# Kernel tuning notes

Measured on AMD Instinct MI355X. Metric: run time of the kernel, lower is better.

The kernel has to match this reference:

```python
import jax, jax.numpy as jnp
import numpy as np

N_NODES = 50000
N_EDGES = 1600000
N_GRAPHS = 128
IN_C, HID, N_CLS = 128, 256, 10


def setup_inputs() -> dict:
    key = jax.random.key(0)
    ks = jax.random.split(key, 8)
    x = jax.random.normal(ks[0], (N_NODES, IN_C), dtype=jnp.float32)
    edge_index = jax.random.randint(ks[1], (2, N_EDGES), 0, N_NODES, dtype=jnp.int64)
    batch = jnp.sort(jax.random.randint(ks[2], (N_NODES,), 0, N_GRAPHS, dtype=jnp.int64))
    def glorot(k, shape):
        lim = np.sqrt(6.0 / (shape[0] + shape[1]))
        return jax.random.uniform(k, shape, jnp.float32, -lim, lim)
    return {
        "x": x, "edge_index": edge_index, "batch": batch,
        "W1": glorot(ks[3], (IN_C, HID)), "b1": jnp.zeros((HID,), jnp.float32),
        "W2": glorot(ks[4], (HID, HID)), "b2": jnp.zeros((HID,), jnp.float32),
        "Wl1": glorot(ks[5], (HID, 64)), "bl1": jnp.zeros((64,), jnp.float32),
        "Wl2": glorot(ks[6], (64, N_CLS)), "bl2": jnp.zeros((N_CLS,), jnp.float32),
    }


def _gcn_conv(x, row, col, deg_inv_sqrt, W, b):
    h = x @ W                                  # [N, out]
    norm = deg_inv_sqrt[row] * deg_inv_sqrt[col]   # [E]
    msg = h[row] * norm[:, None]                   # gather + scale
    agg = jax.ops.segment_sum(msg, col, num_segments=x.shape[0])
    agg = agg + h * (deg_inv_sqrt * deg_inv_sqrt)[:, None]  # self-loop term (norm = 1/deg)
    return agg + b


def reference(x, edge_index, batch, W1, b1, W2, b2, Wl1, bl1, Wl2, bl2):
    N = x.shape[0]
    row, col = edge_index[0], edge_index[1]
    # degree including self-loop, computed on target nodes (PyG convention)
    deg = jax.ops.segment_sum(jnp.ones((row.shape[0],), x.dtype), col, num_segments=N) + 1.0
    deg_inv_sqrt = jax.lax.rsqrt(deg)

    h = jax.nn.relu(_gcn_conv(x, row, col, deg_inv_sqrt, W1, b1))
    h = jax.nn.relu(_gcn_conv(h, row, col, deg_inv_sqrt, W2, b2))

    # global_mean_pool over batch ids
    sums = jax.ops.segment_sum(h, batch, num_segments=N_GRAPHS)
    cnts = jax.ops.segment_sum(jnp.ones((N,), h.dtype), batch, num_segments=N_GRAPHS)
    g = sums / jnp.maximum(cnts, 1.0)[:, None]     # [G, HID]

    g = jax.nn.relu(g @ Wl1 + bl1)
    return jax.nn.log_softmax(g @ Wl2 + bl2, axis=1)
```

## Files before the change

### kernel.cpp

```cpp
#include <hip/hip_runtime.h>
#include <hip/hip_bf16.h>
#include <math.h>

#define NN 50000
#define NG 128
#define INC 128
#define HIDC 256
#define NCLS 10

#define NBLK 256
#define BSH 8
#define NB 196

typedef __attribute__((ext_vector_type(8))) short s8_t;
typedef __attribute__((ext_vector_type(4))) float f4_t;

__device__ inline f4_t mfma16(s8_t a, s8_t b, f4_t c) {
  return __builtin_amdgcn_mfma_f32_16x16x32_bf16(a, b, c, 0, 0, 0);
}

__device__ inline float bf2f(ushort u) {
  union { unsigned int i; float f; } c; c.i = ((unsigned int)u) << 16; return c.f;
}
__device__ inline ushort f2bf(float f) {
  __hip_bfloat16 h = __float2bfloat16(f);
  return *(ushort*)&h;
}

__device__ inline void gload_lds16(const void* g, void* l) {
  __builtin_amdgcn_global_load_lds(
      (const __attribute__((address_space(1))) unsigned int*)g,
      (__attribute__((address_space(3))) unsigned int*)l, 16, 0, 0);
}

__global__ __launch_bounds__(256) void edge_hist(const int* __restrict__ ecol,
                                                 int* __restrict__ hist, int E, int chunk) {
  __shared__ int h[NB];
  int blk = blockIdx.x;
  for (int i = threadIdx.x; i < NB; i += 256) h[i] = 0;
  __syncthreads();
  int e0 = blk * chunk, e1 = min(e0 + chunk, E);
  for (int e = e0 + threadIdx.x; e < e1; e += 256)
    atomicAdd(&h[ecol[e] >> BSH], 1);
  __syncthreads();
  for (int i = threadIdx.x; i < NB; i += 256) hist[i * NBLK + blk] = h[i];
}

__global__ __launch_bounds__(256) void edge_partition(const int* __restrict__ erow,
                                                      const int* __restrict__ ecol,
                                                      const int* __restrict__ histBase,
                                                      unsigned* __restrict__ part,
                                                      int E, int chunk) {
  __shared__ int cur[NB];
  int blk = blockIdx.x;
  for (int i = threadIdx.x; i < NB; i += 256) cur[i] = histBase[i * NBLK + blk];
  __syncthreads();
  int e0 = blk * chunk, e1 = min(e0 + chunk, E);
  for (int e = e0 + threadIdx.x; e < e1; e += 256) {
    int c = ecol[e];
    int b = c >> BSH;
    int pos = atomicAdd(&cur[b], 1);
    part[pos] = ((unsigned)erow[e] << 8) | (unsigned)(c & 255);
  }
}

__global__ __launch_bounds__(256) void bucket_deg_dis(const unsigned* __restrict__ part,
                                                      const int* __restrict__ histBase,
                                                      int* __restrict__ deg,
                                                      float* __restrict__ dis, int N) {
  __shared__ int cnt[256];
  int b = blockIdx.x;
  cnt[threadIdx.x] = 0;
  __syncthreads();
  int s0 = histBase[b * NBLK];
  int s1 = histBase[(b + 1) * NBLK];
  for (int e = s0 + threadIdx.x; e < s1; e += 256)
    atomicAdd(&cnt[part[e] & 255], 1);
  __syncthreads();
  int node = (b << BSH) + threadIdx.x;
  if (node < N) {
    int d = cnt[threadIdx.x];
    deg[node] = d;
    dis[node] = rsqrtf((float)d + 1.0f);
  }
}

__global__ __launch_bounds__(256) void bucket_csr(const unsigned* __restrict__ part,
                                                  const int* __restrict__ histBase,
                                                  const int* __restrict__ offsets,
                                                  int* __restrict__ rows_csr, int N) {
  __shared__ int cur[256];
  int b = blockIdx.x;
  int node = (b << BSH) + threadIdx.x;
  cur[threadIdx.x] = (node < N) ? offsets[node] : 0;
  __syncthreads();
  int s0 = histBase[b * NBLK];
  int s1 = histBase[(b + 1) * NBLK];
  for (int e = s0 + threadIdx.x; e < s1; e += 256) {
    unsigned pv = part[e];
    int pos = atomicAdd(&cur[pv & 255], 1);
    rows_csr[pos] = (int)(pv >> 8);
  }
}

#define SCAN_T 256
#define SCAN_V 8
#define SCAN_VPB (SCAN_T * SCAN_V)

__global__ __launch_bounds__(SCAN_T) void scanA(const int* __restrict__ deg,
                                                int* __restrict__ offsets,
                                                int* __restrict__ blockTotals, int n) {
  __shared__ int sm[SCAN_T];
  int b = blockIdx.x;
  int t = threadIdx.x;
  int base = b * SCAN_VPB + t * SCAN_V;
  int v[SCAN_V];
  int run = 0;
  #pragma unroll
  for (int j = 0; j < SCAN_V; ++j) {
    int idx = base + j;
    int d = (idx < n) ? deg[idx] : 0;
    run += d;
    v[j] = run;
  }
  sm[t] = run;
  __syncthreads();
  #pragma unroll
  for (int off = 1; off < SCAN_T; off <<= 1) {
    int x = (t >= off) ? sm[t - off] : 0;
    __syncthreads();
    sm[t] += x;
    __syncthreads();
  }
  int excl = (t == 0) ? 0 : sm[t - 1];
  #pragma unroll
  for (int j = 0; j < SCAN_V; ++j) {
    int idx = base + j;
    if (idx < n) offsets[idx + 1] = v[j] + excl;
  }
  if (t == SCAN_T - 1) blockTotals[b] = sm[t];
}

__global__ void scanB(int* __restrict__ blockTotals, int nb) {
  if (threadIdx.x == 0 && blockIdx.x == 0) {
    int run = 0;
    for (int i = 0; i < nb; ++i) {
      int v = blockTotals[i];
      blockTotals[i] = run;
      run += v;
    }
  }
}

__global__ void scanC(int* __restrict__ offsets, const int* __restrict__ blockTotals, int n) {
  int stride = gridDim.x * blockDim.x;
  for (int i = blockIdx.x * blockDim.x + threadIdx.x; i < n; i += stride) {
    offsets[i + 1] += blockTotals[i / SCAN_VPB];
    if (i == 0) offsets[0] = 0;
  }
}

__global__ void cast_f32_bf16(const float* __restrict__ in, ushort* __restrict__ out, int n4) {
  int i = blockIdx.x * blockDim.x + threadIdx.x;
  if (i < n4) {
    float4 v = ((const float4*)in)[i];
    ushort4 o;
    o.x = f2bf(v.x); o.y = f2bf(v.y); o.z = f2bf(v.z); o.w = f2bf(v.w);
    ((ushort4*)out)[i] = o;
  }
}

__global__ void transpose_cast2(const float* __restrict__ W1, ushort* __restrict__ W1T,
                                const float* __restrict__ W2, ushort* __restrict__ W2T) {
  int idx = blockIdx.x * blockDim.x + threadIdx.x;
  if (idx < INC * HIDC) {
    int k = idx / HIDC, n = idx % HIDC;
    W1T[(long)n * INC + k] = f2bf(W1[idx]);
  }
  int i2 = idx - INC * HIDC;
  if (i2 >= 0 && i2 < HIDC * HIDC) {
    int k = i2 / HIDC, n = i2 % HIDC;
    W2T[(long)n * HIDC + k] = f2bf(W2[i2]);
  }
}

__global__ __launch_bounds__(256) void aggregate128_bf16(
    const ushort* __restrict__ xb, const float* __restrict__ dis,
    const int* __restrict__ offsets, const int* __restrict__ rows_csr,
    ushort* __restrict__ outb, int N) {
  int node = blockIdx.x * 4 + (threadIdx.x >> 6);
  if (node >= N) return;
  int lane = threadIdx.x & 63;
  float di = dis[node];
  const unsigned int* xv = (const unsigned int*)xb;
  unsigned int sv = xv[(long)node * 64 + lane];
  float a0 = bf2f((ushort)sv) * di * di;
  float a1 = bf2f((ushort)(sv >> 16)) * di * di;
  int e0 = offsets[node], e1 = offsets[node + 1];
  int e = e0;
  for (; e + 3 < e1; e += 4) {
    int r0 = rows_csr[e], r1 = rows_csr[e + 1];
    int r2 = rows_csr[e + 2], r3 = rows_csr[e + 3];
    float s0 = dis[r0] * di, s1 = dis[r1] * di;
    float s2 = dis[r2] * di, s3 = dis[r3] * di;
    unsigned int v0 = xv[(long)r0 * 64 + lane];
    unsigned int v1 = xv[(long)r1 * 64 + lane];
    unsigned int v2 = xv[(long)r2 * 64 + lane];
    unsigned int v3 = xv[(long)r3 * 64 + lane];
    a0 = fmaf(bf2f((ushort)v0), s0, a0); a1 = fmaf(bf2f((ushort)(v0 >> 16)), s0, a1);
    a0 = fmaf(bf2f((ushort)v1), s1, a0); a1 = fmaf(bf2f((ushort)(v1 >> 16)), s1, a1);
    a0 = fmaf(bf2f((ushort)v2), s2, a0); a1 = fmaf(bf2f((ushort)(v2 >> 16)), s2, a1);
    a0 = fmaf(bf2f((ushort)v3), s3, a0); a1 = fmaf(bf2f((ushort)(v3 >> 16)), s3, a1);
  }
  for (; e < e1; ++e) {
    int r0 = rows_csr[e];
    float s0 = dis[r0] * di;
    unsigned int v0 = xv[(long)r0 * 64 + lane];
    a0 = fmaf(bf2f((ushort)v0), s0, a0); a1 = fmaf(bf2f((ushort)(v0 >> 16)), s0, a1);
  }
  unsigned int o = (unsigned int)f2bf(a0) | ((unsigned int)f2bf(a1) << 16);
  ((unsigned int*)outb)[(long)node * 64 + lane] = o;
}

__global__ __launch_bounds__(256) void aggregate256_bf16(
    const ushort* __restrict__ xb, const float* __restrict__ dis,
    const int* __restrict__ offsets, const int* __restrict__ rows_csr,
    ushort* __restrict__ outb, int N) {
  int node = blockIdx.x * 4 + (threadIdx.x >> 6);
  if (node >= N) return;
  int lane = threadIdx.x & 63;
  float di = dis[node];
  const uint2* xv = (const uint2*)xb;
  uint2 sv = xv[(long)node * 64 + lane];
  float a0 = bf2f((ushort)sv.x) * di * di;
  float a1 = bf2f((ushort)(sv.x >> 16)) * di * di;
  float a2 = bf2f((ushort)sv.y) * di * di;
  float a3 = bf2f((ushort)(sv.y >> 16)) * di * di;
  int e0 = offsets[node], e1 = offsets[node + 1];
  int e = e0;
  for (; e + 3 < e1; e += 4) {
    int r0 = rows_csr[e], r1 = rows_csr[e + 1];
    int r2 = rows_csr[e + 2], r3 = rows_csr[e + 3];
    float s0 = dis[r0] * di, s1 = dis[r1] * di;
    float s2 = dis[r2] * di, s3 = dis[r3] * di;
    uint2 v0 = xv[(long)r0 * 64 + lane];
    uint2 v1 = xv[(long)r1 * 64 + lane];
    uint2 v2 = xv[(long)r2 * 64 + lane];
    uint2 v3 = xv[(long)r3 * 64 + lane];
    a0 = fmaf(bf2f((ushort)v0.x), s0, a0); a1 = fmaf(bf2f((ushort)(v0.x >> 16)), s0, a1);
    a2 = fmaf(bf2f((ushort)v0.y), s0, a2); a3 = fmaf(bf2f((ushort)(v0.y >> 16)), s0, a3);
    a0 = fmaf(bf2f((ushort)v1.x), s1, a0); a1 = fmaf(bf2f((ushort)(v1.x >> 16)), s1, a1);
    a2 = fmaf(bf2f((ushort)v1.y), s1, a2); a3 = fmaf(bf2f((ushort)(v1.y >> 16)), s1, a3);
    a0 = fmaf(bf2f((ushort)v2.x), s2, a0); a1 = fmaf(bf2f((ushort)(v2.x >> 16)), s2, a1);
    a2 = fmaf(bf2f((ushort)v2.y), s2, a2); a3 = fmaf(bf2f((ushort)(v2.y >> 16)), s2, a3);
    a0 = fmaf(bf2f((ushort)v3.x), s3, a0); a1 = fmaf(bf2f((ushort)(v3.x >> 16)), s3, a1);
    a2 = fmaf(bf2f((ushort)v3.y), s3, a2); a3 = fmaf(bf2f((ushort)(v3.y >> 16)), s3, a3);
  }
  for (; e < e1; ++e) {
    int r0 = rows_csr[e];
    float s0 = dis[r0] * di;
    uint2 v0 = xv[(long)r0 * 64 + lane];
    a0 = fmaf(bf2f((ushort)v0.x), s0, a0); a1 = fmaf(bf2f((ushort)(v0.x >> 16)), s0, a1);
    a2 = fmaf(bf2f((ushort)v0.y), s0, a2); a3 = fmaf(bf2f((ushort)(v0.y >> 16)), s0, a3);
  }
  uint2 o;
  o.x = (unsigned int)f2bf(a0) | ((unsigned int)f2bf(a1) << 16);
  o.y = (unsigned int)f2bf(a2) | ((unsigned int)f2bf(a3) << 16);
  ((uint2*)outb)[(long)node * 64 + lane] = o;
}

template <int K>
__global__ __launch_bounds__(256) void gemm_mfma(
    const ushort* __restrict__ A, const ushort* __restrict__ WT,
    const float* __restrict__ bias, ushort* __restrict__ outb, int M) {
  __shared__ ushort smem[24576];
  const int tid = threadIdx.x;
  const int lane = tid & 63;
  const int wave = tid >> 6;
  const int wm = wave >> 1, wn = wave & 1;
  const int m0 = blockIdx.x * 128;

  f4_t acc[4][8] = {};

  for (int k0 = 0; k0 < K; k0 += 64) {
    __syncthreads();
    #pragma unroll
    for (int is = 0; is < 4; ++is) {
      int s = is * 256 + tid;
      int row = s >> 3;
      int ch = (s & 7) ^ (row & 7);
      long grow = m0 + row; if (grow > M - 1) grow = M - 1;
      gload_lds16(A + grow * K + k0 + ch * 8, &smem[(is * 256 + wave * 64) * 8]);
    }
    #pragma unroll
    for (int ib = 0; ib < 8; ++ib) {
      int s = ib * 256 + tid;
      int row = s >> 3;
      int ch = (s & 7) ^ (row & 7);
      gload_lds16(WT + (long)row * K + k0 + ch * 8,
                  &smem[8192 + (ib * 256 + wave * 64) * 8]);
    }
    asm volatile("s_waitcnt vmcnt(0)" ::: "memory");
    __syncthreads();
    #pragma unroll
    for (int ks = 0; ks < 2; ++ks) {
      s8_t af[4];
      #pragma unroll
      for (int mi = 0; mi < 4; ++mi) {
        int row = wm * 64 + mi * 16 + (lane & 15);
        int ch = (ks * 4 + (lane >> 4)) ^ (row & 7);
        af[mi] = *(const s8_t*)(&smem[row * 64 + ch * 8]);
      }
      #pragma unroll
      for (int ni = 0; ni < 8; ++ni) {
        int brow = wn * 128 + ni * 16 + (lane & 15);
        int ch = (ks * 4 + (lane >> 4)) ^ (brow & 7);
        s8_t bf = *(const s8_t*)(&smem[8192 + brow * 64 + ch * 8]);
        #pragma unroll
        for (int mi = 0; mi < 4; ++mi)
          acc[mi][ni] = mfma16(af[mi], bf, acc[mi][ni]);
      }
    }
  }
  #pragma unroll
  for (int ni = 0; ni < 8; ++ni) {
    int col = wn * 128 + ni * 16 + (lane & 15);
    float bb = bias[col];
    #pragma unroll
    for (int mi = 0; mi < 4; ++mi) {
      #pragma unroll
      for (int r = 0; r < 4; ++r) {
        int row = m0 + wm * 64 + mi * 16 + (lane >> 4) * 4 + r;
        if (row < M) {
          float v = fmaxf(acc[mi][ni][r] + bb, 0.0f);
          outb[(long)row * HIDC + col] = f2bf(v);
        }
      }
    }
  }
}

__global__ void find_bounds(const int* __restrict__ batch, int* __restrict__ gstart, int n) {
  int stride = gridDim.x * blockDim.x;
  for (int i = blockIdx.x * blockDim.x + threadIdx.x; i < n; i += stride) {
    int b = batch[i];
    if (i == 0) {
      for (int g = 0; g <= b; ++g) gstart[g] = 0;
    } else {
      int pb = batch[i - 1];
      if (pb != b)
        for (int g = pb + 1; g <= b; ++g) gstart[g] = i;
    }
    if (i == n - 1) {
      for (int g = b + 1; g <= NG; ++g) gstart[g] = n;
    }
  }
}

#define POOL_SPLIT 8
__global__ __launch_bounds__(HIDC) void pool_range_bf16(const ushort* __restrict__ h,
                                                        const int* __restrict__ gstart,
                                                        float* __restrict__ gsum) {
  int g = blockIdx.x;
  int s = blockIdx.y;
  int c = threadIdx.x;
  int s0 = gstart[g], s1 = gstart[g + 1];
  int len = s1 - s0;
  int chunk = (len + POOL_SPLIT - 1) / POOL_SPLIT;
  int i0 = s0 + s * chunk;
  int i1 = min(i0 + chunk, s1);
  float acc = 0.0f;
  for (int i = i0; i < i1; ++i) acc += bf2f(h[(long)i * HIDC + c]);
  if (i1 > i0) atomicAdd(&gsum[g * HIDC + c], acc);
}

__global__ __launch_bounds__(64) void mlp_kernel(
    const float* __restrict__ gsum, const int* __restrict__ gstart,
    const float* __restrict__ Wl1, const float* __restrict__ bl1,
    const float* __restrict__ Wl2, const float* __restrict__ bl2,
    float* __restrict__ out) {
  __shared__ float g[HIDC];
  __shared__ float hid[64];
  __shared__ float logits[NCLS];
  __shared__ float red[2];
  int i = blockIdx.x;
  int t = threadIdx.x;
  int cnt = gstart[i + 1] - gstart[i];
  float inv = 1.0f / fmaxf((float)cnt, 1.0f);
  for (int c = t; c < HIDC; c += 64) g[c] = gsum[i * HIDC + c] * inv;
  __syncthreads();
  float acc = bl1[t];
  for (int c = 0; c < HIDC; ++c) acc = fmaf(g[c], Wl1[c * 64 + t], acc);
  hid[t] = fmaxf(acc, 0.0f);
  __syncthreads();
  if (t < NCLS) {
    float l = bl2[t];
    for (int c = 0; c < 64; ++c) l = fmaf(hid[c], Wl2[c * NCLS + t], l);
    logits[t] = l;
  }
  __syncthreads();
  if (t == 0) {
    float m = -1e30f;
    for (int k = 0; k < NCLS; ++k) m = fmaxf(m, logits[k]);
    float s = 0.f;
    for (int k = 0; k < NCLS; ++k) s += expf(logits[k] - m);
    red[0] = m;
    red[1] = logf(s);
  }
  __syncthreads();
  if (t < NCLS) out[i * NCLS + t] = logits[t] - red[0] - red[1];
}

extern "C" void kernel_launch(void* const* d_in, const int* in_sizes, int n_in,
                              void* d_out, int out_size, void* d_ws, size_t ws_size,
                              hipStream_t stream) {
  const float* x = (const float*)d_in[0];
  const int* edge_index = (const int*)d_in[1];
  const int* batch = (const int*)d_in[2];
  const float* W1 = (const float*)d_in[3];
  const float* b1 = (const float*)d_in[4];
  const float* W2 = (const float*)d_in[5];
  const float* b2 = (const float*)d_in[6];
  const float* Wl1 = (const float*)d_in[7];
  const float* bl1 = (const float*)d_in[8];
  const float* Wl2 = (const float*)d_in[9];
  const float* bl2 = (const float*)d_in[10];
  float* out = (float*)d_out;

  const int N = in_sizes[0] / INC;
  const int E = in_sizes[1] / 2;
  const int* erow = edge_index;
  const int* ecol = edge_index + E;

  char* p = (char*)d_ws;
  auto alloc = [&](size_t bytes) {
    void* r = (void*)p;
    p += (bytes + 255) & ~(size_t)255;
    return r;
  };
  int* deg = (int*)alloc((size_t)N * 4);
  float* dis = (float*)alloc((size_t)N * 4);
  int* offsets = (int*)alloc((size_t)(N + 1) * 4);
  int* rows_csr = (int*)alloc((size_t)E * 4);
  unsigned* part = (unsigned*)alloc((size_t)E * 4);
  int* hist = (int*)alloc((size_t)(NB * NBLK) * 4);
  int* histBase = (int*)alloc((size_t)(NB * NBLK + 1) * 4);
  float* gsum = (float*)alloc((size_t)NG * HIDC * 4);
  int* gstart = (int*)alloc((size_t)(NG + 1) * 4);
  int* blockTotals = (int*)alloc((size_t)256 * 4);
  ushort* W1T = (ushort*)alloc((size_t)INC * HIDC * 2);
  ushort* W2T = (ushort*)alloc((size_t)HIDC * HIDC * 2);
  ushort* xb = (ushort*)alloc((size_t)N * INC * 2);
  ushort* agg1b = (ushort*)alloc((size_t)N * INC * 2);
  ushort* h1b = (ushort*)alloc((size_t)N * HIDC * 2);
  ushort* agg2b = (ushort*)alloc((size_t)N * HIDC * 2);
  ushort* h2b = xb;

  hipMemsetAsync(gsum, 0, (size_t)NG * HIDC * 4, stream);

  const int chunk = (E + NBLK - 1) / NBLK;
  edge_hist<<<NBLK, 256, 0, stream>>>(ecol, hist, E, chunk);
  {
    const int nh = NB * NBLK;
    const int nbh = (nh + SCAN_VPB - 1) / SCAN_VPB;
    scanA<<<nbh, SCAN_T, 0, stream>>>(hist, histBase, blockTotals, nh);
    scanB<<<1, 64, 0, stream>>>(blockTotals, nbh);
    scanC<<<(nh + 255) / 256, 256, 0, stream>>>(histBase, blockTotals, nh);
  }
  edge_partition<<<NBLK, 256, 0, stream>>>(erow, ecol, histBase, part, E, chunk);
  bucket_deg_dis<<<NB, 256, 0, stream>>>(part, histBase, deg, dis, N);
  {
    const int nb = (N + SCAN_VPB - 1) / SCAN_VPB;
    scanA<<<nb, SCAN_T, 0, stream>>>(deg, offsets, blockTotals, N);
    scanB<<<1, 64, 0, stream>>>(blockTotals, nb);
    scanC<<<(N + 255) / 256, 256, 0, stream>>>(offsets, blockTotals, N);
  }
  bucket_csr<<<NB, 256, 0, stream>>>(part, histBase, offsets, rows_csr, N);

  cast_f32_bf16<<<(N * INC / 4 + 255) / 256, 256, 0, stream>>>(x, xb, N * INC / 4);
  {
    int tot = INC * HIDC + HIDC * HIDC;
    transpose_cast2<<<(tot + 255) / 256, 256, 0, stream>>>(W1, W1T, W2, W2T);
  }

  aggregate128_bf16<<<(N + 3) / 4, 256, 0, stream>>>(xb, dis, offsets, rows_csr, agg1b, N);
  gemm_mfma<INC><<<(N + 127) / 128, 256, 0, stream>>>(agg1b, W1T, b1, h1b, N);
  aggregate256_bf16<<<(N + 3) / 4, 256, 0, stream>>>(h1b, dis, offsets, rows_csr, agg2b, N);
  gemm_mfma<HIDC><<<(N + 127) / 128, 256, 0, stream>>>(agg2b, W2T, b2, h2b, N);
  find_bounds<<<(N + 255) / 256, 256, 0, stream>>>(batch, gstart, N);
  {
    dim3 pgrid(NG, POOL_SPLIT);
    pool_range_bf16<<<pgrid, HIDC, 0, stream>>>(h2b, gstart, gsum);
  }
  mlp_kernel<<<NG, 64, 0, stream>>>(gsum, gstart, Wl1, bl1, Wl2, bl2, out);
}
```

Measured before the change: 435.0 us.

## Use column-blocked feature layout so aggregation gathers fit in cache per slice

Features are stored in 32-column blocks (column-block major), so each aggregation pass processes one 64-byte slice per node across a grid.y dimension. Within a wave, four 16-lane groups split the edges and combine with shuffles. The aim is a smaller per-slice working set for better L2 reuse of the random gathers. The GEMM is also split over N into 128-column tiles with a smaller LDS footprint and reads or writes the blocked layout. The trade-off is more passes over the CSR indices and dis array, plus 64-byte gathers per edge instead of full rows.

```diff
diff --git a/kernel.cpp b/kernel.cpp
--- a/kernel.cpp
+++ b/kernel.cpp
@@ -25,6 +25,9 @@
 __device__ inline ushort f2bf(float f) {
   __hip_bfloat16 h = __float2bfloat16(f);
   return *(ushort*)&h;
+}
+__device__ inline unsigned packbf(float a, float b) {
+  return (unsigned)f2bf(a) | ((unsigned)f2bf(b) << 16);
 }
 
 __device__ inline void gload_lds16(const void* g, void* l) {
@@ -160,14 +163,13 @@
   }
 }
 
-__global__ void cast_f32_bf16(const float* __restrict__ in, ushort* __restrict__ out, int n4) {
-  int i = blockIdx.x * blockDim.x + threadIdx.x;
-  if (i < n4) {
-    float4 v = ((const float4*)in)[i];
-    ushort4 o;
-    o.x = f2bf(v.x); o.y = f2bf(v.y); o.z = f2bf(v.z); o.w = f2bf(v.w);
-    ((ushort4*)out)[i] = o;
-  }
+__global__ void cast_x_cb(const float* __restrict__ x, unsigned* __restrict__ xcb, int N) {
+  int t = blockIdx.x * 256 + threadIdx.x;
+  if (t >= N * 64) return;
+  int n = t >> 6, pp = t & 63;
+  float v0 = x[(long)n * 128 + 2 * pp];
+  float v1 = x[(long)n * 128 + 2 * pp + 1];
+  xcb[((long)(pp >> 4) * N + n) * 16 + (pp & 15)] = packbf(v0, v1);
 }
 
 __global__ void transpose_cast2(const float* __restrict__ W1, ushort* __restrict__ W1T,
@@ -184,103 +186,49 @@
   }
 }
 
-__global__ __launch_bounds__(256) void aggregate128_bf16(
-    const ushort* __restrict__ xb, const float* __restrict__ dis,
+__global__ __launch_bounds__(256) void aggregate_cb(
+    const unsigned* __restrict__ xcb, const float* __restrict__ dis,
     const int* __restrict__ offsets, const int* __restrict__ rows_csr,
-    ushort* __restrict__ outb, int N) {
+    unsigned* __restrict__ outcb, int N) {
   int node = blockIdx.x * 4 + (threadIdx.x >> 6);
   if (node >= N) return;
   int lane = threadIdx.x & 63;
+  int g = lane >> 4;
+  int cl = lane & 15;
+  long cbN = (long)blockIdx.y * N;
   float di = dis[node];
-  const unsigned int* xv = (const unsigned int*)xb;
-  unsigned int sv = xv[(long)node * 64 + lane];
-  float a0 = bf2f((ushort)sv) * di * di;
-  float a1 = bf2f((ushort)(sv >> 16)) * di * di;
+  float a0 = 0.0f, a1 = 0.0f;
+  if (g == 0) {
+    unsigned sv = xcb[(cbN + node) * 16 + cl];
+    a0 = bf2f((ushort)sv) * di * di;
+    a1 = bf2f((ushort)(sv >> 16)) * di * di;
+  }
   int e0 = offsets[node], e1 = offsets[node + 1];
-  int e = e0;
-  for (; e + 3 < e1; e += 4) {
-    int r0 = rows_csr[e], r1 = rows_csr[e + 1];
-    int r2 = rows_csr[e + 2], r3 = rows_csr[e + 3];
-    float s0 = dis[r0] * di, s1 = dis[r1] * di;
-    float s2 = dis[r2] * di, s3 = dis[r3] * di;
-    unsigned int v0 = xv[(long)r0 * 64 + lane];
-    unsigned int v1 = xv[(long)r1 * 64 + lane];
-    unsigned int v2 = xv[(long)r2 * 64 + lane];
-    unsigned int v3 = xv[(long)r3 * 64 + lane];
-    a0 = fmaf(bf2f((ushort)v0), s0, a0); a1 = fmaf(bf2f((ushort)(v0 >> 16)), s0, a1);
-    a0 = fmaf(bf2f((ushort)v1), s1, a0); a1 = fmaf(bf2f((ushort)(v1 >> 16)), s1, a1);
-    a0 = fmaf(bf2f((ushort)v2), s2, a0); a1 = fmaf(bf2f((ushort)(v2 >> 16)), s2, a1);
-    a0 = fmaf(bf2f((ushort)v3), s3, a0); a1 = fmaf(bf2f((ushort)(v3 >> 16)), s3, a1);
-  }
-  for (; e < e1; ++e) {
-    int r0 = rows_csr[e];
-    float s0 = dis[r0] * di;
-    unsigned int v0 = xv[(long)r0 * 64 + lane];
-    a0 = fmaf(bf2f((ushort)v0), s0, a0); a1 = fmaf(bf2f((ushort)(v0 >> 16)), s0, a1);
-  }
-  unsigned int o = (unsigned int)f2bf(a0) | ((unsigned int)f2bf(a1) << 16);
-  ((unsigned int*)outb)[(long)node * 64 + lane] = o;
-}
-
-__global__ __launch_bounds__(256) void aggregate256_bf16(
-    const ushort* __restrict__ xb, const float* __restrict__ dis,
-    const int* __restrict__ offsets, const int* __restrict__ rows_csr,
-    ushort* __restrict__ outb, int N) {
-  int node = blockIdx.x * 4 + (threadIdx.x >> 6);
-  if (node >= N) return;
-  int lane = threadIdx.x & 63;
-  float di = dis[node];
-  const uint2* xv = (const uint2*)xb;
-  uint2 sv = xv[(long)node * 64 + lane];
-  float a0 = bf2f((ushort)sv.x) * di * di;
-  float a1 = bf2f((ushort)(sv.x >> 16)) * di * di;
-  float a2 = bf2f((ushort)sv.y) * di * di;
-  float a3 = bf2f((ushort)(sv.y >> 16)) * di * di;
-  int e0 = offsets[node], e1 = offsets[node + 1];
-  int e = e0;
-  for (; e + 3 < e1; e += 4) {
-    int r0 = rows_csr[e], r1 = rows_csr[e + 1];
-    int r2 = rows_csr[e + 2], r3 = rows_csr[e + 3];
-    float s0 = dis[r0] * di, s1 = dis[r1] * di;
-    float s2 = dis[r2] * di, s3 = dis[r3] * di;
-    uint2 v0 = xv[(long)r0 * 64 + lane];
-    uint2 v1 = xv[(long)r1 * 64 + lane];
-    uint2 v2 = xv[(long)r2 * 64 + lane];
-    uint2 v3 = xv[(long)r3 * 64 + lane];
-    a0 = fmaf(bf2f((ushort)v0.x), s0, a0); a1 = fmaf(bf2f((ushort)(v0.x >> 16)), s0, a1);
-    a2 = fmaf(bf2f((ushort)v0.y), s0, a2); a3 = fmaf(bf2f((ushort)(v0.y >> 16)), s0, a3);
-    a0 = fmaf(bf2f((ushort)v1.x), s1, a0); a1 = fmaf(bf2f((ushort)(v1.x >> 16)), s1, a1);
-    a2 = fmaf(bf2f((ushort)v1.y), s1, a2); a3 = fmaf(bf2f((ushort)(v1.y >> 16)), s1, a3);
-    a0 = fmaf(bf2f((ushort)v2.x), s2, a0); a1 = fmaf(bf2f((ushort)(v2.x >> 16)), s2, a1);
-    a2 = fmaf(bf2f((ushort)v2.y), s2, a2); a3 = fmaf(bf2f((ushort)(v2.y >> 16)), s2, a3);
-    a0 = fmaf(bf2f((ushort)v3.x), s3, a0); a1 = fmaf(bf2f((ushort)(v3.x >> 16)), s3, a1);
-    a2 = fmaf(bf2f((ushort)v3.y), s3, a2); a3 = fmaf(bf2f((ushort)(v3.y >> 16)), s3, a3);
-  }
-  for (; e < e1; ++e) {
-    int r0 = rows_csr[e];
-    float s0 = dis[r0] * di;
-    uint2 v0 = xv[(long)r0 * 64 + lane];
-    a0 = fmaf(bf2f((ushort)v0.x), s0, a0); a1 = fmaf(bf2f((ushort)(v0.x >> 16)), s0, a1);
-    a2 = fmaf(bf2f((ushort)v0.y), s0, a2); a3 = fmaf(bf2f((ushort)(v0.y >> 16)), s0, a3);
-  }
-  uint2 o;
-  o.x = (unsigned int)f2bf(a0) | ((unsigned int)f2bf(a1) << 16);
-  o.y = (unsigned int)f2bf(a2) | ((unsigned int)f2bf(a3) << 16);
-  ((uint2*)outb)[(long)node * 64 + lane] = o;
-}
-
-template <int K>
+  for (int e = e0 + g; e < e1; e += 4) {
+    int src = rows_csr[e];
+    float s = dis[src] * di;
+    unsigned v = xcb[(cbN + src) * 16 + cl];
+    a0 = fmaf(bf2f((ushort)v), s, a0);
+    a1 = fmaf(bf2f((ushort)(v >> 16)), s, a1);
+  }
+  a0 += __shfl_xor(a0, 16); a0 += __shfl_xor(a0, 32);
+  a1 += __shfl_xor(a1, 16); a1 += __shfl_xor(a1, 32);
+  if (lane < 16) outcb[(cbN + node) * 16 + cl] = packbf(a0, a1);
+}
+
+template <int K, bool OUTCB>
 __global__ __launch_bounds__(256) void gemm_mfma(
     const ushort* __restrict__ A, const ushort* __restrict__ WT,
     const float* __restrict__ bias, ushort* __restrict__ outb, int M) {
-  __shared__ ushort smem[24576];
+  __shared__ ushort smem[16384];
   const int tid = threadIdx.x;
   const int lane = tid & 63;
   const int wave = tid >> 6;
   const int wm = wave >> 1, wn = wave & 1;
   const int m0 = blockIdx.x * 128;
-
-  f4_t acc[4][8] = {};
+  const int n0 = blockIdx.y * 128;
+
+  f4_t acc[4][4] = {};
 
   for (int k0 = 0; k0 < K; k0 += 64) {
     __syncthreads();
@@ -289,22 +237,24 @@
       int s = is * 256 + tid;
       int row = s >> 3;
       int ch = (s & 7) ^ (row & 7);
+      int k = k0 + ch * 8;
       long grow = m0 + row; if (grow > M - 1) grow = M - 1;
-      gload_lds16(A + grow * K + k0 + ch * 8, &smem[(is * 256 + wave * 64) * 8]);
+      const ushort* g = A + ((long)(k >> 5) * M + grow) * 32 + (k & 31);
+      gload_lds16(g, &smem[(is * 256 + wave * 64) * 8]);
     }
     #pragma unroll
-    for (int ib = 0; ib < 8; ++ib) {
-      int s = ib * 256 + tid;
+    for (int is = 0; is < 4; ++is) {
+      int s = is * 256 + tid;
       int row = s >> 3;
       int ch = (s & 7) ^ (row & 7);
-      gload_lds16(WT + (long)row * K + k0 + ch * 8,
-                  &smem[8192 + (ib * 256 + wave * 64) * 8]);
+      const ushort* g = WT + (long)(n0 + row) * K + k0 + ch * 8;
+      gload_lds16(g, &smem[8192 + (is * 256 + wave * 64) * 8]);
     }
     asm volatile("s_waitcnt vmcnt(0)" ::: "memory");
     __syncthreads();
     #pragma unroll
     for (int ks = 0; ks < 2; ++ks) {
-      s8_t af[4];
+      s8_t af[4], bfr[4];
       #pragma unroll
       for (int mi = 0; mi < 4; ++mi) {
         int row = wm * 64 + mi * 16 + (lane & 15);
@@ -312,19 +262,21 @@
         af[mi] = *(const s8_t*)(&smem[row * 64 + ch * 8]);
       }
       #pragma unroll
-      for (int ni = 0; ni < 8; ++ni) {
-        int brow = wn * 128 + ni * 16 + (lane & 15);
-        int ch = (ks * 4 + (lane >> 4)) ^ (brow & 7);
-        s8_t bf = *(const s8_t*)(&smem[8192 + brow * 64 + ch * 8]);
+      for (int ni = 0; ni < 4; ++ni) {
+        int row = wn * 64 + ni * 16 + (lane & 15);
+        int ch = (ks * 4 + (lane >> 4)) ^ (row & 7);
+        bfr[ni] = *(const s8_t*)(&smem[8192 + row * 64 + ch * 8]);
+      }
+      #pragma unroll
+      for (int mi = 0; mi < 4; ++mi)
         #pragma unroll
-        for (int mi = 0; mi < 4; ++mi)
-          acc[mi][ni] = mfma16(af[mi], bf, acc[mi][ni]);
-      }
+        for (int ni = 0; ni < 4; ++ni)
+          acc[mi][ni] = mfma16(af[mi], bfr[ni], acc[mi][ni]);
     }
   }
   #pragma unroll
-  for (int ni = 0; ni < 8; ++ni) {
-    int col = wn * 128 + ni * 16 + (lane & 15);
+  for (int ni = 0; ni < 4; ++ni) {
+    int col = n0 + wn * 64 + ni * 16 + (lane & 15);
     float bb = bias[col];
     #pragma unroll
     for (int mi = 0; mi < 4; ++mi) {
@@ -333,7 +285,10 @@
         int row = m0 + wm * 64 + mi * 16 + (lane >> 4) * 4 + r;
         if (row < M) {
           float v = fmaxf(acc[mi][ni][r] + bb, 0.0f);
-          outb[(long)row * HIDC + col] = f2bf(v);
+          if (OUTCB)
+            outb[((long)(col >> 5) * M + row) * 32 + (col & 31)] = f2bf(v);
+          else
+            outb[(long)row * HIDC + col] = f2bf(v);
         }
       }
     }
@@ -450,11 +405,11 @@
   int* blockTotals = (int*)alloc((size_t)256 * 4);
   ushort* W1T = (ushort*)alloc((size_t)INC * HIDC * 2);
   ushort* W2T = (ushort*)alloc((size_t)HIDC * HIDC * 2);
-  ushort* xb = (ushort*)alloc((size_t)N * INC * 2);
-  ushort* agg1b = (ushort*)alloc((size_t)N * INC * 2);
-  ushort* h1b = (ushort*)alloc((size_t)N * HIDC * 2);
-  ushort* agg2b = (ushort*)alloc((size_t)N * HIDC * 2);
-  ushort* h2b = xb;
+  unsigned* x_cb = (unsigned*)alloc((size_t)N * INC * 2);
+  unsigned* agg1_cb = (unsigned*)alloc((size_t)N * INC * 2);
+  unsigned* h1_cb = (unsigned*)alloc((size_t)N * HIDC * 2);
+  unsigned* agg2_cb = (unsigned*)alloc((size_t)N * HIDC * 2);
+  ushort* h2 = (ushort*)x_cb;
 
   hipMemsetAsync(gsum, 0, (size_t)NG * HIDC * 4, stream);
 
@@ -477,20 +432,34 @@
   }
   bucket_csr<<<NB, 256, 0, stream>>>(part, histBase, offsets, rows_csr, N);
 
-  cast_f32_bf16<<<(N * INC / 4 + 255) / 256, 256, 0, stream>>>(x, xb, N * INC / 4);
+  cast_x_cb<<<(N * 64 + 255) / 256, 256, 0, stream>>>(x, x_cb, N);
   {
     int tot = INC * HIDC + HIDC * HIDC;
     transpose_cast2<<<(tot + 255) / 256, 256, 0, stream>>>(W1, W1T, W2, W2T);
   }
 
-  aggregate128_bf16<<<(N + 3) / 4, 256, 0, stream>>>(xb, dis, offsets, rows_csr, agg1b, N);
-  gemm_mfma<INC><<<(N + 127) / 128, 256, 0, stream>>>(agg1b, W1T, b1, h1b, N);
-  aggregate256_bf16<<<(N + 3) / 4, 256, 0, stream>>>(h1b, dis, offsets, rows_csr, agg2b, N);
-  gemm_mfma<HIDC><<<(N + 127) / 128, 256, 0, stream>>>(agg2b, W2T, b2, h2b, N);
+  {
+    dim3 agrid((N + 3) / 4, INC / 32);
+    aggregate_cb<<<agrid, 256, 0, stream>>>(x_cb, dis, offsets, rows_csr, agg1_cb, N);
+  }
+  {
+    dim3 grid((N + 127) / 128, HIDC / 128);
+    gemm_mfma<INC, true><<<grid, 256, 0, stream>>>(
+        (const ushort*)agg1_cb, W1T, b1, (ushort*)h1_cb, N);
+  }
+  {
+    dim3 agrid((N + 3) / 4, HIDC / 32);
+    aggregate_cb<<<agrid, 256, 0, stream>>>(h1_cb, dis, offsets, rows_csr, agg2_cb, N);
+  }
+  {
+    dim3 grid((N + 127) / 128, HIDC / 128);
+    gemm_mfma<HIDC, false><<<grid, 256, 0, stream>>>(
+        (const ushort*)agg2_cb, W2T, b2, h2, N);
+  }
   find_bounds<<<(N + 255) / 256, 256, 0, stream>>>(batch, gstart, N);
   {
     dim3 pgrid(NG, POOL_SPLIT);
-    pool_range_bf16<<<pgrid, HIDC, 0, stream>>>(h2b, gstart, gsum);
+    pool_range_bf16<<<pgrid, HIDC, 0, stream>>>(h2, gstart, gsum);
   }
   mlp_kernel<<<NG, 64, 0, stream>>>(gsum, gstart, Wl1, bl1, Wl2, bl2, out);
 }
```

Measured after the change: 813.3 us. 1.87x slower.
